# Optimization experiments

Hardware: AMD Instinct MI355X
Metric: run time of the kernel (lower is better)

The kernel has to match this reference:

```python
import jax, jax.numpy as jnp
import numpy as np

N = 65536      # points per cloud
L = 64         # voxel grid side
K_KNN = 16


def _decode(lin):
    x = lin // (L * L); y = (lin // L) % L; z = lin % L
    return np.stack([x, y, z], -1).astype(np.int32)


def _build_nbr(out_c, in_c, r):
    # Minkowski-style kernel map: for each output coord and each of (2r+1)^3
    # offsets, index of matching input coord, sentinel=len(in_c) if absent.
    g = np.arange(-r, r + 1)
    offs = np.stack(np.meshgrid(g, g, g, indexing='ij'), -1).reshape(-1, 3)
    S = 80  # encode side (coords in [-r, L+r) shifted by 8 fit in [0,80))
    def enc(c):
        return ((c[..., 0].astype(np.int64) + 8) * S + (c[..., 1] + 8)) * S + (c[..., 2] + 8)
    kin = enc(in_c)
    order = np.argsort(kin).astype(np.int32)
    skin = kin[order]
    nin = len(in_c)
    rows = []
    for i in range(0, len(out_c), 8192):
        q = out_c[i:i + 8192, None, :] + offs[None]
        kq = enc(q).reshape(-1)
        pos = np.clip(np.searchsorted(skin, kq), 0, nin - 1)
        ok = skin[pos] == kq
        rows.append(np.where(ok, order[pos], nin).astype(np.int32).reshape(-1, len(offs)))
    return np.concatenate(rows, 0)


def _knn(qc, rc, k):
    # brute-force knn (matches pytorch3d.ops.knn_points indices up to order;
    # downstream mean/softmax are permutation invariant)
    q = qc.astype(np.float32); r = rc.astype(np.float32)
    rn = (r * r).sum(1)
    out = []
    for i in range(0, len(q), 4096):
        qb = q[i:i + 4096]
        d = (qb * qb).sum(1)[:, None] + rn[None, :] - 2.0 * qb @ r.T
        out.append(np.argpartition(d, k, axis=1)[:, :k].astype(np.int32))
    return np.concatenate(out, 0)


def setup_inputs():
    rng = np.random.default_rng(0)
    prev_C = _decode(rng.permutation(L ** 3)[:N])
    cur_C = _decode(rng.permutation(L ** 3)[:N])
    nbr_interp = _build_nbr(cur_C, prev_C, 4)  # 9^3 = 729 offsets
    nbr3 = _build_nbr(cur_C, cur_C, 1)         # 3^3 = 27 offsets
    knn_idx = _knn(cur_C, prev_C, K_KNN)
    key = jax.random.key(0)
    ks = jax.random.split(key, 32)
    f32 = jnp.float32
    def w(k, shape, s):
        return jax.random.normal(k, shape, f32) * s
    C = 32
    return dict(
        prev_F=w(ks[0], (N, 1), 1.0),
        prev_C=jnp.asarray(prev_C), cur_C=jnp.asarray(cur_C),
        nbr_interp=jnp.asarray(nbr_interp), nbr3=jnp.asarray(nbr3),
        knn_idx=jnp.asarray(knn_idx),
        W_interp=w(ks[1], (729, 1, 1), 0.05), b_interp=w(ks[2], (1,), 0.05),
        W_conv0=w(ks[3], (27, 2, C), 0.1), b_conv0=w(ks[4], (C,), 0.05),
        W_conv1=w(ks[5], (C, C), 0.1), b_conv1=w(ks[6], (C,), 0.05),
        Wi00=w(ks[7], (C, C // 4), 0.1), bi00=w(ks[8], (C // 4,), 0.05),
        Wi01=w(ks[9], (27, C // 4, C // 4), 0.1), bi01=w(ks[10], (C // 4,), 0.05),
        Wi02=w(ks[11], (C // 4, C // 2), 0.1), bi02=w(ks[12], (C // 2,), 0.05),
        Wi10=w(ks[13], (27, C, C // 4), 0.1), bi10=w(ks[14], (C // 4,), 0.05),
        Wi11=w(ks[15], (27, C // 4, C // 2), 0.1), bi11=w(ks[16], (C // 2,), 0.05),
        Wq=w(ks[17], (1, 1), 0.5), bq=w(ks[18], (1,), 0.1),
        Wk=w(ks[19], (4, 1), 0.5), bk=w(ks[20], (1,), 0.1),
        Wv=w(ks[21], (4, 1), 0.5), bv=w(ks[22], (1,), 0.1),
        Wlin=w(ks[23], (1, 1), 0.5), blin=w(ks[24], (1,), 0.1),
        ln1_g=jnp.ones((1,), f32), ln1_b=jnp.zeros((1,), f32),
        ln2_g=jnp.ones((1,), f32), ln2_b=jnp.zeros((1,), f32),
    )


def _sparse_conv(feats, nbr, W, b):
    # gather-GEMM-scatter sparse conv; sentinel index == len(feats) -> zero row
    fpad = jnp.concatenate([feats, jnp.zeros((1, feats.shape[1]), feats.dtype)], 0)
    g = fpad[nbr]  # [Nout, K, Cin]
    return jnp.einsum('nkc,kcd->nd', g, W) + b


def _ln(x, g, b, eps=1e-5):
    m = jnp.mean(x, -1, keepdims=True)
    v = jnp.var(x, -1, keepdims=True)
    return (x - m) * jax.lax.rsqrt(v + eps) * g + b


def reference(prev_F, prev_C, cur_C, nbr_interp, nbr3, knn_idx,
              W_interp, b_interp, W_conv0, b_conv0, W_conv1, b_conv1,
              Wi00, bi00, Wi01, bi01, Wi02, bi02, Wi10, bi10, Wi11, bi11,
              Wq, bq, Wk, bk, Wv, bv, Wlin, blin, ln1_g, ln1_b, ln2_g, ln2_b):
    # interp: generative 9^3 sparse conv from previous coords onto current coords
    context = _sparse_conv(prev_F, nbr_interp, W_interp, b_interp)  # [N,1]

    # Target_Point_Transformer_Last (channels = in_channels = 1, head=1, k=16)
    pxyz = prev_C.astype(jnp.float32)
    cxyz = cur_C.astype(jnp.float32)
    knn_xyz = pxyz[knn_idx] - cxyz[:, None, :]          # [N,16,3]
    knn_xyz = knn_xyz / jnp.max(knn_xyz)                # global-max normalization
    knn_feat = prev_F[knn_idx]                          # [N,16,1]
    x = jnp.mean(knn_feat, axis=1)                      # init_feature [N,1]
    nf = jnp.concatenate([knn_feat, knn_xyz], axis=2)   # [N,16,4]
    Q = (x @ Wq + bq)[:, None, :]                       # [N,1,1] (head=1)
    Kt = (nf @ Wk + bk)[:, None, :, :]                  # [N,1,16,1]
    V = (nf @ Wv + bv)[:, None, :, :]
    att = jnp.einsum('nhd,nhkd->nhk', Q, Kt) / 1.0      # d = sqrt(channels=1)
    att = jax.nn.softmax(att, axis=-1)
    af = jnp.einsum('nhk,nhkd->nhd', att, V).reshape(-1, 1)
    x1 = x + af
    x1 = _ln(x1, ln1_g, ln1_b)
    x1 = x1 + x1 @ Wlin + blin
    interp_feat = _ln(x1, ln2_g, ln2_b)                 # [N,1]

    ctx = jnp.concatenate([context, interp_feat], axis=-1)  # [N,2]
    h = jax.nn.relu(_sparse_conv(ctx, nbr3, W_conv0, b_conv0))  # [N,32]
    # InceptionResNet
    o = jax.nn.relu(h @ Wi00 + bi00)                         # 1x1 conv [N,8]
    o0 = jax.nn.relu(_sparse_conv(o, nbr3, Wi01, bi01))
    o0 = jax.nn.relu(o0 @ Wi02 + bi02)                       # [N,16]
    o1 = jax.nn.relu(_sparse_conv(h, nbr3, Wi10, bi10))
    o1 = jax.nn.relu(_sparse_conv(o1, nbr3, Wi11, bi11))     # [N,16]
    blk = jnp.concatenate([o0, o1], axis=-1) + h
    out = jax.nn.relu(blk) @ W_conv1 + b_conv1               # 1x1 conv [N,32]
    return out
```

## Files before the change

kernel.cpp:

```cpp
#include <hip/hip_runtime.h>


#define NPTS 65536
#define GD 72
#define GSX (GD*GD)
#define GRID_FLOATS (GD*GD*GD)
#define CD 64
#define CELLS (CD*CD*CD)

__global__ __launch_bounds__(256) void k_scatter(const float* __restrict__ prev_F,
                                                 const int* __restrict__ prev_C,
                                                 const int* __restrict__ cur_C,
                                                 float* __restrict__ gridF,
                                                 int* __restrict__ pidg) {
    int m = blockIdx.x * 256 + threadIdx.x;
    int x = prev_C[m*3+0], y = prev_C[m*3+1], z = prev_C[m*3+2];
    gridF[(x+4)*GSX + (y+4)*GD + (z+4)] = prev_F[m];
    int cx = cur_C[m*3+0], cy = cur_C[m*3+1], cz = cur_C[m*3+2];
    pidg[(cx*CD + cy)*CD + cz] = m;
}

__global__ __launch_bounds__(256) void k_ctx_dense(const float* __restrict__ gridF,
                                                   const int* __restrict__ pidg,
                                                   const float* __restrict__ W_interp,
                                                   const float* __restrict__ b_interp,
                                                   float* __restrict__ ctx) {
    __shared__ float tile[16*16*24];
    int bid = blockIdx.x;
    int bx = (bid >> 5) * 8, by = ((bid >> 2) & 7) * 8, bz = (bid & 3) * 16;
    int t = threadIdx.x;
    for (int i = t; i < 16*16*24; i += 256) {
        int a = i / (16*24);
        int r = i - a*(16*24);
        int b = r / 24;
        int c = r - b*24;
        tile[i] = gridF[(bx + a)*GSX + (by + b)*GD + (bz + c)];
    }
    __syncthreads();
    int tz = (t & 3) * 4;
    int ty = (t >> 2) & 7;
    int tx = t >> 5;
    float acc0 = 0.f, acc1 = 0.f, acc2 = 0.f, acc3 = 0.f;
    for (int dx = 0; dx < 9; ++dx) {
        for (int dy = 0; dy < 9; ++dy) {
            const float* row = &tile[((tx + dx)*16 + (ty + dy))*24 + tz];
            float4 r0 = *(const float4*)(row);
            float4 r1 = *(const float4*)(row + 4);
            float4 r2 = *(const float4*)(row + 8);
            float v[12] = {r0.x,r0.y,r0.z,r0.w, r1.x,r1.y,r1.z,r1.w, r2.x,r2.y,r2.z,r2.w};
            const float* wp = &W_interp[(dx*9 + dy)*9];
            #pragma unroll
            for (int dz = 0; dz < 9; ++dz) {
                float w = wp[dz];
                acc0 = fmaf(v[dz+0], w, acc0);
                acc1 = fmaf(v[dz+1], w, acc1);
                acc2 = fmaf(v[dz+2], w, acc2);
                acc3 = fmaf(v[dz+3], w, acc3);
            }
        }
    }
    float bi = b_interp[0];
    int cell = ((bx + tx)*CD + (by + ty))*CD + (bz + tz);
    int4 pids = *(const int4*)(pidg + cell);
    if (pids.x >= 0) ctx[pids.x] = acc0 + bi;
    if (pids.y >= 0) ctx[pids.y] = acc1 + bi;
    if (pids.z >= 0) ctx[pids.z] = acc2 + bi;
    if (pids.w >= 0) ctx[pids.w] = acc3 + bi;
}

__global__ __launch_bounds__(256) void k_conv0(const int* __restrict__ nbr3,
                                               const float* __restrict__ ctx,
                                               const float* __restrict__ W_conv0,
                                               const float* __restrict__ b_conv0,
                                               const float* __restrict__ Wi00,
                                               const float* __restrict__ bi00,
                                               float* __restrict__ h,
                                               float* __restrict__ o) {
    __shared__ int ln[256*27];
    int n0 = blockIdx.x * 256;
    for (int i = threadIdx.x; i < 256*27; i += 256) ln[i] = nbr3[n0*27 + i];
    __syncthreads();
    int n = n0 + threadIdx.x;
    float acc[32];
    #pragma unroll
    for (int d = 0; d < 32; ++d) acc[d] = b_conv0[d];
    for (int k = 0; k < 27; ++k) {
        int idx = ln[threadIdx.x*27 + k];
        float cv = 0.f;
        if (idx < NPTS) cv = ctx[idx];
        #pragma unroll
        for (int d = 0; d < 32; ++d)
            acc[d] = fmaf(cv, W_conv0[k*64 + d], acc[d]);
    }
    #pragma unroll
    for (int d = 0; d < 32; ++d) acc[d] = fmaxf(acc[d], 0.f);
    float4* hp = (float4*)(h + (size_t)n*32);
    #pragma unroll
    for (int q = 0; q < 8; ++q) hp[q] = make_float4(acc[q*4], acc[q*4+1], acc[q*4+2], acc[q*4+3]);
    float ov[8];
    #pragma unroll
    for (int j = 0; j < 8; ++j) {
        float t = bi00[j];
        #pragma unroll
        for (int d = 0; d < 32; ++d) t = fmaf(acc[d], Wi00[d*8 + j], t);
        ov[j] = fmaxf(t, 0.f);
    }
    float4* op = (float4*)(o + (size_t)n*8);
    op[0] = make_float4(ov[0], ov[1], ov[2], ov[3]);
    op[1] = make_float4(ov[4], ov[5], ov[6], ov[7]);
}

__global__ __launch_bounds__(256) void k_mid(const int* __restrict__ nbr3,
                                             const float* __restrict__ h,
                                             const float* __restrict__ o,
                                             const float* __restrict__ Wi01,
                                             const float* __restrict__ bi01,
                                             const float* __restrict__ Wi10,
                                             const float* __restrict__ bi10,
                                             float* __restrict__ o0a,
                                             float* __restrict__ o1a) {
    __shared__ int ln[256*27];
    int n0 = blockIdx.x * 256;
    for (int i = threadIdx.x; i < 256*27; i += 256) ln[i] = nbr3[n0*27 + i];
    __syncthreads();
    int n = n0 + threadIdx.x;
    float a0[8], a1[8];
    #pragma unroll
    for (int j = 0; j < 8; ++j) { a0[j] = bi01[j]; a1[j] = bi10[j]; }
    for (int k = 0; k < 27; ++k) {
        int idx = ln[threadIdx.x*27 + k];
        if (idx < NPTS) {
            const float4* orow = (const float4*)(o + (size_t)idx*8);
            float4 oa = orow[0], ob = orow[1];
            float oc[8] = {oa.x, oa.y, oa.z, oa.w, ob.x, ob.y, ob.z, ob.w};
            #pragma unroll
            for (int c = 0; c < 8; ++c)
                #pragma unroll
                for (int j = 0; j < 8; ++j)
                    a0[j] = fmaf(oc[c], Wi01[(k*8+c)*8 + j], a0[j]);
            const float4* hrow = (const float4*)(h + (size_t)idx*32);
            #pragma unroll
            for (int q = 0; q < 8; ++q) {
                float4 hv = hrow[q];
                float hc[4] = {hv.x, hv.y, hv.z, hv.w};
                #pragma unroll
                for (int c = 0; c < 4; ++c)
                    #pragma unroll
                    for (int j = 0; j < 8; ++j)
                        a1[j] = fmaf(hc[c], Wi10[(k*32 + q*4 + c)*8 + j], a1[j]);
            }
        }
    }
    float4* p0 = (float4*)(o0a + (size_t)n*8);
    p0[0] = make_float4(fmaxf(a0[0],0.f), fmaxf(a0[1],0.f), fmaxf(a0[2],0.f), fmaxf(a0[3],0.f));
    p0[1] = make_float4(fmaxf(a0[4],0.f), fmaxf(a0[5],0.f), fmaxf(a0[6],0.f), fmaxf(a0[7],0.f));
    float4* p1 = (float4*)(o1a + (size_t)n*8);
    p1[0] = make_float4(fmaxf(a1[0],0.f), fmaxf(a1[1],0.f), fmaxf(a1[2],0.f), fmaxf(a1[3],0.f));
    p1[1] = make_float4(fmaxf(a1[4],0.f), fmaxf(a1[5],0.f), fmaxf(a1[6],0.f), fmaxf(a1[7],0.f));
}

__global__ __launch_bounds__(256) void k_out(const int* __restrict__ nbr3,
                                             const float* __restrict__ h,
                                             const float* __restrict__ o0a,
                                             const float* __restrict__ o1a,
                                             const float* __restrict__ Wi11,
                                             const float* __restrict__ bi11,
                                             const float* __restrict__ Wi02,
                                             const float* __restrict__ bi02,
                                             const float* __restrict__ W_conv1,
                                             const float* __restrict__ b_conv1,
                                             float* __restrict__ out) {
    __shared__ int ln[256*27];
    int n0 = blockIdx.x * 256;
    for (int i = threadIdx.x; i < 256*27; i += 256) ln[i] = nbr3[n0*27 + i];
    __syncthreads();
    int n = n0 + threadIdx.x;
    float a1[16];
    #pragma unroll
    for (int j = 0; j < 16; ++j) a1[j] = bi11[j];
    for (int k = 0; k < 27; ++k) {
        int idx = ln[threadIdx.x*27 + k];
        if (idx < NPTS) {
            const float4* row = (const float4*)(o1a + (size_t)idx*8);
            float4 ra = row[0], rb = row[1];
            float rc[8] = {ra.x, ra.y, ra.z, ra.w, rb.x, rb.y, rb.z, rb.w};
            #pragma unroll
            for (int c = 0; c < 8; ++c)
                #pragma unroll
                for (int j = 0; j < 16; ++j)
                    a1[j] = fmaf(rc[c], Wi11[(k*8+c)*16 + j], a1[j]);
        }
    }
    float blk[32];
    {
        const float4* prow = (const float4*)(o0a + (size_t)n*8);
        float4 pa = prow[0], pb = prow[1];
        float pc[8] = {pa.x, pa.y, pa.z, pa.w, pb.x, pb.y, pb.z, pb.w};
        #pragma unroll
        for (int j = 0; j < 16; ++j) {
            float t = bi02[j];
            #pragma unroll
            for (int c = 0; c < 8; ++c) t = fmaf(pc[c], Wi02[c*16 + j], t);
            blk[j] = fmaxf(t, 0.f);
        }
    }
    #pragma unroll
    for (int j = 0; j < 16; ++j) blk[16+j] = fmaxf(a1[j], 0.f);
    const float4* hrow4 = (const float4*)(h + (size_t)n*32);
    #pragma unroll
    for (int q = 0; q < 8; ++q) {
        float4 hv = hrow4[q];
        blk[q*4+0] += hv.x; blk[q*4+1] += hv.y; blk[q*4+2] += hv.z; blk[q*4+3] += hv.w;
    }
    #pragma unroll
    for (int e = 0; e < 32; ++e) blk[e] = fmaxf(blk[e], 0.f);
    float acc[32];
    #pragma unroll
    for (int d = 0; d < 32; ++d) acc[d] = b_conv1[d];
    #pragma unroll
    for (int e = 0; e < 32; ++e)
        #pragma unroll
        for (int d = 0; d < 32; ++d)
            acc[d] = fmaf(blk[e], W_conv1[e*32 + d], acc[d]);
    float4* outp = (float4*)(out + (size_t)n*32);
    #pragma unroll
    for (int q = 0; q < 8; ++q) outp[q] = make_float4(acc[q*4], acc[q*4+1], acc[q*4+2], acc[q*4+3]);
}

extern "C" void kernel_launch(void* const* d_in, const int* in_sizes, int n_in,
                              void* d_out, int out_size, void* d_ws, size_t ws_size,
                              hipStream_t stream) {
    (void)in_sizes; (void)n_in; (void)out_size; (void)ws_size;
    const float* prev_F   = (const float*)d_in[0];
    const int*   prev_C   = (const int*)d_in[1];
    const int*   cur_C    = (const int*)d_in[2];
    const int*   nbr3     = (const int*)d_in[4];
    const float* W_interp = (const float*)d_in[6];
    const float* b_interp = (const float*)d_in[7];
    const float* W_conv0  = (const float*)d_in[8];
    const float* b_conv0  = (const float*)d_in[9];
    const float* W_conv1  = (const float*)d_in[10];
    const float* b_conv1  = (const float*)d_in[11];
    const float* Wi00     = (const float*)d_in[12];
    const float* bi00     = (const float*)d_in[13];
    const float* Wi01     = (const float*)d_in[14];
    const float* bi01     = (const float*)d_in[15];
    const float* Wi02     = (const float*)d_in[16];
    const float* bi02     = (const float*)d_in[17];
    const float* Wi10     = (const float*)d_in[18];
    const float* bi10     = (const float*)d_in[19];
    const float* Wi11     = (const float*)d_in[20];
    const float* bi11     = (const float*)d_in[21];

    float* ws    = (float*)d_ws;
    float* gridF = ws;
    int*   pidg  = (int*)(ws + 373248);
    float* ctx   = ws + 635392;
    float* h     = ws + 700928;
    float* o     = ws + 2798080;
    float* o0a   = ws + 3322368;
    float* o1a   = ws + 3846656;
    float* outp  = (float*)d_out;

    hipMemsetAsync(gridF, 0,    GRID_FLOATS*sizeof(float), stream);
    hipMemsetAsync(pidg,  0xFF, CELLS*sizeof(int),         stream);
    k_scatter  <<<NPTS/256, 256, 0, stream>>>(prev_F, prev_C, cur_C, gridF, pidg);
    k_ctx_dense<<<256,      256, 0, stream>>>(gridF, pidg, W_interp, b_interp, ctx);
    k_conv0    <<<NPTS/256, 256, 0, stream>>>(nbr3, ctx, W_conv0, b_conv0, Wi00, bi00, h, o);
    k_mid      <<<NPTS/256, 256, 0, stream>>>(nbr3, h, o, Wi01, bi01, Wi10, bi10, o0a, o1a);
    k_out      <<<NPTS/256, 256, 0, stream>>>(nbr3, h, o0a, o1a, Wi11, bi11, Wi02, bi02, W_conv1, b_conv1, outp);
}
```

Baseline: 447.8 us.

## Split sparse-conv kernel taps across waves and shrink dense-context tiles

The dense context kernel now uses 8x8x8 output blocks with 2 outputs per thread, doubling the block count. The three sparse-conv kernels now process 64 points per block, each of four waves taking 7 of the 27 kernel taps. Partial sums are reduced through shared memory, and k_mid double-buffers its neighbour row loads. The goal is more parallelism and memory-level parallelism on the gathers, at the cost of extra shared-memory reductions, a barrier, and idle waves during the epilogue.

```diff
diff --git a/kernel.cpp b/kernel.cpp
--- a/kernel.cpp
+++ b/kernel.cpp
@@ -25,48 +25,46 @@
                                                    const float* __restrict__ W_interp,
                                                    const float* __restrict__ b_interp,
                                                    float* __restrict__ ctx) {
-    __shared__ float tile[16*16*24];
+    __shared__ float tile[16*16*16];
     int bid = blockIdx.x;
-    int bx = (bid >> 5) * 8, by = ((bid >> 2) & 7) * 8, bz = (bid & 3) * 16;
+    int bx = (bid >> 6) * 8, by = ((bid >> 3) & 7) * 8, bz = (bid & 7) * 8;
     int t = threadIdx.x;
-    for (int i = t; i < 16*16*24; i += 256) {
-        int a = i / (16*24);
-        int r = i - a*(16*24);
-        int b = r / 24;
-        int c = r - b*24;
+    #pragma unroll
+    for (int rep = 0; rep < 16; ++rep) {
+        int i = t + rep*256;
+        int a = i >> 8, b = (i >> 4) & 15, c = i & 15;
         tile[i] = gridF[(bx + a)*GSX + (by + b)*GD + (bz + c)];
     }
     __syncthreads();
-    int tz = (t & 3) * 4;
+    int tz = (t & 3) * 2;
     int ty = (t >> 2) & 7;
     int tx = t >> 5;
-    float acc0 = 0.f, acc1 = 0.f, acc2 = 0.f, acc3 = 0.f;
+    float acc0 = 0.f, acc1 = 0.f;
     for (int dx = 0; dx < 9; ++dx) {
         for (int dy = 0; dy < 9; ++dy) {
-            const float* row = &tile[((tx + dx)*16 + (ty + dy))*24 + tz];
-            float4 r0 = *(const float4*)(row);
-            float4 r1 = *(const float4*)(row + 4);
-            float4 r2 = *(const float4*)(row + 8);
-            float v[12] = {r0.x,r0.y,r0.z,r0.w, r1.x,r1.y,r1.z,r1.w, r2.x,r2.y,r2.z,r2.w};
+            const float* row = &tile[((tx + dx)*16 + (ty + dy))*16 + tz];
+            float2 r0 = *(const float2*)(row);
+            float2 r1 = *(const float2*)(row + 2);
+            float2 r2 = *(const float2*)(row + 4);
+            float2 r3 = *(const float2*)(row + 6);
+            float2 r4 = *(const float2*)(row + 8);
+            float v[10] = {r0.x,r0.y,r1.x,r1.y,r2.x,r2.y,r3.x,r3.y,r4.x,r4.y};
             const float* wp = &W_interp[(dx*9 + dy)*9];
             #pragma unroll
             for (int dz = 0; dz < 9; ++dz) {
                 float w = wp[dz];
                 acc0 = fmaf(v[dz+0], w, acc0);
                 acc1 = fmaf(v[dz+1], w, acc1);
-                acc2 = fmaf(v[dz+2], w, acc2);
-                acc3 = fmaf(v[dz+3], w, acc3);
             }
         }
     }
     float bi = b_interp[0];
     int cell = ((bx + tx)*CD + (by + ty))*CD + (bz + tz);
-    int4 pids = *(const int4*)(pidg + cell);
+    int2 pids = *(const int2*)(pidg + cell);
     if (pids.x >= 0) ctx[pids.x] = acc0 + bi;
     if (pids.y >= 0) ctx[pids.y] = acc1 + bi;
-    if (pids.z >= 0) ctx[pids.z] = acc2 + bi;
-    if (pids.w >= 0) ctx[pids.w] = acc3 + bi;
-}
+}
+
 
 __global__ __launch_bounds__(256) void k_conv0(const int* __restrict__ nbr3,
                                                const float* __restrict__ ctx,
@@ -76,38 +74,51 @@
                                                const float* __restrict__ bi00,
                                                float* __restrict__ h,
                                                float* __restrict__ o) {
-    __shared__ int ln[256*27];
-    int n0 = blockIdx.x * 256;
-    for (int i = threadIdx.x; i < 256*27; i += 256) ln[i] = nbr3[n0*27 + i];
-    __syncthreads();
-    int n = n0 + threadIdx.x;
-    float acc[32];
-    #pragma unroll
-    for (int d = 0; d < 32; ++d) acc[d] = b_conv0[d];
-    for (int k = 0; k < 27; ++k) {
-        int idx = ln[threadIdx.x*27 + k];
-        float cv = 0.f;
-        if (idx < NPTS) cv = ctx[idx];
+    __shared__ float part[3][32][64];
+    int lane = threadIdx.x & 63;
+    int q    = threadIdx.x >> 6;
+    int kbase = __builtin_amdgcn_readfirstlane(q * 7);
+    int n = blockIdx.x * 64 + lane;
+    float cv[7];
+    #pragma unroll
+    for (int j = 0; j < 7; ++j) {
+        int k = kbase + j;
+        int raw = (k < 27) ? nbr3[(size_t)n*27 + k] : NPTS;
+        cv[j] = (raw < NPTS) ? ctx[raw < NPTS ? raw : 0] : 0.f;
+    }
+    float ac[32];
+    #pragma unroll
+    for (int d = 0; d < 32; ++d) ac[d] = (q == 0) ? b_conv0[d] : 0.f;
+    #pragma unroll
+    for (int j = 0; j < 7; ++j) {
+        const float* wr = &W_conv0[(kbase + j)*64];
+        #pragma unroll
+        for (int d = 0; d < 32; ++d) ac[d] = fmaf(cv[j], wr[d], ac[d]);
+    }
+    if (q > 0) {
+        #pragma unroll
+        for (int d = 0; d < 32; ++d) part[q-1][d][lane] = ac[d];
+    }
+    __syncthreads();
+    if (q == 0) {
         #pragma unroll
         for (int d = 0; d < 32; ++d)
-            acc[d] = fmaf(cv, W_conv0[k*64 + d], acc[d]);
-    }
-    #pragma unroll
-    for (int d = 0; d < 32; ++d) acc[d] = fmaxf(acc[d], 0.f);
-    float4* hp = (float4*)(h + (size_t)n*32);
-    #pragma unroll
-    for (int q = 0; q < 8; ++q) hp[q] = make_float4(acc[q*4], acc[q*4+1], acc[q*4+2], acc[q*4+3]);
-    float ov[8];
-    #pragma unroll
-    for (int j = 0; j < 8; ++j) {
-        float t = bi00[j];
-        #pragma unroll
-        for (int d = 0; d < 32; ++d) t = fmaf(acc[d], Wi00[d*8 + j], t);
-        ov[j] = fmaxf(t, 0.f);
-    }
-    float4* op = (float4*)(o + (size_t)n*8);
-    op[0] = make_float4(ov[0], ov[1], ov[2], ov[3]);
-    op[1] = make_float4(ov[4], ov[5], ov[6], ov[7]);
+            ac[d] = fmaxf(ac[d] + part[0][d][lane] + part[1][d][lane] + part[2][d][lane], 0.f);
+        float4* hp = (float4*)(h + (size_t)n*32);
+        #pragma unroll
+        for (int w = 0; w < 8; ++w) hp[w] = make_float4(ac[w*4], ac[w*4+1], ac[w*4+2], ac[w*4+3]);
+        float ov[8];
+        #pragma unroll
+        for (int j = 0; j < 8; ++j) {
+            float tt = bi00[j];
+            #pragma unroll
+            for (int d = 0; d < 32; ++d) tt = fmaf(ac[d], Wi00[d*8 + j], tt);
+            ov[j] = fmaxf(tt, 0.f);
+        }
+        float4* op = (float4*)(o + (size_t)n*8);
+        op[0] = make_float4(ov[0], ov[1], ov[2], ov[3]);
+        op[1] = make_float4(ov[4], ov[5], ov[6], ov[7]);
+    }
 }
 
 __global__ __launch_bounds__(256) void k_mid(const int* __restrict__ nbr3,
@@ -119,44 +130,70 @@
                                              const float* __restrict__ bi10,
                                              float* __restrict__ o0a,
                                              float* __restrict__ o1a) {
-    __shared__ int ln[256*27];
-    int n0 = blockIdx.x * 256;
-    for (int i = threadIdx.x; i < 256*27; i += 256) ln[i] = nbr3[n0*27 + i];
-    __syncthreads();
-    int n = n0 + threadIdx.x;
-    float a0[8], a1[8];
-    #pragma unroll
-    for (int j = 0; j < 8; ++j) { a0[j] = bi01[j]; a1[j] = bi10[j]; }
-    for (int k = 0; k < 27; ++k) {
-        int idx = ln[threadIdx.x*27 + k];
-        if (idx < NPTS) {
-            const float4* orow = (const float4*)(o + (size_t)idx*8);
-            float4 oa = orow[0], ob = orow[1];
-            float oc[8] = {oa.x, oa.y, oa.z, oa.w, ob.x, ob.y, ob.z, ob.w};
-            #pragma unroll
-            for (int c = 0; c < 8; ++c)
+    __shared__ float part[3][16][64];
+    int lane = threadIdx.x & 63;
+    int q    = threadIdx.x >> 6;
+    int kbase = __builtin_amdgcn_readfirstlane(q * 7);
+    int n = blockIdx.x * 64 + lane;
+    const float4 z4 = make_float4(0.f, 0.f, 0.f, 0.f);
+    int  idxs[7]; bool acts[7];
+    #pragma unroll
+    for (int j = 0; j < 7; ++j) {
+        int k = kbase + j;
+        int raw = (k < 27) ? nbr3[(size_t)n*27 + k] : NPTS;
+        acts[j] = raw < NPTS;
+        idxs[j] = acts[j] ? raw : 0;
+    }
+    float ac[16];
+    #pragma unroll
+    for (int d = 0; d < 8; ++d) { ac[d] = (q==0)? bi01[d] : 0.f; ac[8+d] = (q==0)? bi10[d] : 0.f; }
+    float4 bo[2][2], bh[2][8];
+    auto loadtap = [&](int J, int S) {
+        const float4* op_ = (const float4*)(o + (size_t)idxs[J]*8);
+        const float4* hp_ = (const float4*)(h + (size_t)idxs[J]*32);
+        bool a_ = acts[J];
+        bo[S][0] = a_ ? op_[0] : z4;  bo[S][1] = a_ ? op_[1] : z4;
+        #pragma unroll
+        for (int w = 0; w < 8; ++w) bh[S][w] = a_ ? hp_[w] : z4;
+    };
+    loadtap(0, 0);
+    #pragma unroll
+    for (int j = 0; j < 7; ++j) {
+        const int s = j & 1;
+        if (j + 1 < 7) loadtap(j + 1, s ^ 1);
+        float oc[8] = {bo[s][0].x, bo[s][0].y, bo[s][0].z, bo[s][0].w,
+                       bo[s][1].x, bo[s][1].y, bo[s][1].z, bo[s][1].w};
+        const float* w0 = &Wi01[(kbase + j)*64];
+        #pragma unroll
+        for (int c = 0; c < 8; ++c)
+            #pragma unroll
+            for (int d = 0; d < 8; ++d) ac[d] = fmaf(oc[c], w0[c*8 + d], ac[d]);
+        const float* w1 = &Wi10[(kbase + j)*256];
+        #pragma unroll
+        for (int w = 0; w < 8; ++w) {
+            float hc[4] = {bh[s][w].x, bh[s][w].y, bh[s][w].z, bh[s][w].w};
+            #pragma unroll
+            for (int c = 0; c < 4; ++c)
                 #pragma unroll
-                for (int j = 0; j < 8; ++j)
-                    a0[j] = fmaf(oc[c], Wi01[(k*8+c)*8 + j], a0[j]);
-            const float4* hrow = (const float4*)(h + (size_t)idx*32);
-            #pragma unroll
-            for (int q = 0; q < 8; ++q) {
-                float4 hv = hrow[q];
-                float hc[4] = {hv.x, hv.y, hv.z, hv.w};
-                #pragma unroll
-                for (int c = 0; c < 4; ++c)
-                    #pragma unroll
-                    for (int j = 0; j < 8; ++j)
-                        a1[j] = fmaf(hc[c], Wi10[(k*32 + q*4 + c)*8 + j], a1[j]);
-            }
-        }
-    }
-    float4* p0 = (float4*)(o0a + (size_t)n*8);
-    p0[0] = make_float4(fmaxf(a0[0],0.f), fmaxf(a0[1],0.f), fmaxf(a0[2],0.f), fmaxf(a0[3],0.f));
-    p0[1] = make_float4(fmaxf(a0[4],0.f), fmaxf(a0[5],0.f), fmaxf(a0[6],0.f), fmaxf(a0[7],0.f));
-    float4* p1 = (float4*)(o1a + (size_t)n*8);
-    p1[0] = make_float4(fmaxf(a1[0],0.f), fmaxf(a1[1],0.f), fmaxf(a1[2],0.f), fmaxf(a1[3],0.f));
-    p1[1] = make_float4(fmaxf(a1[4],0.f), fmaxf(a1[5],0.f), fmaxf(a1[6],0.f), fmaxf(a1[7],0.f));
+                for (int d = 0; d < 8; ++d) ac[8+d] = fmaf(hc[c], w1[(w*4+c)*8 + d], ac[8+d]);
+        }
+    }
+    if (q > 0) {
+        #pragma unroll
+        for (int d = 0; d < 16; ++d) part[q-1][d][lane] = ac[d];
+    }
+    __syncthreads();
+    if (q == 0) {
+        #pragma unroll
+        for (int d = 0; d < 16; ++d)
+            ac[d] = fmaxf(ac[d] + part[0][d][lane] + part[1][d][lane] + part[2][d][lane], 0.f);
+        float4* p0 = (float4*)(o0a + (size_t)n*8);
+        p0[0] = make_float4(ac[0], ac[1], ac[2],  ac[3]);
+        p0[1] = make_float4(ac[4], ac[5], ac[6],  ac[7]);
+        float4* p1 = (float4*)(o1a + (size_t)n*8);
+        p1[0] = make_float4(ac[8], ac[9], ac[10], ac[11]);
+        p1[1] = make_float4(ac[12],ac[13],ac[14], ac[15]);
+    }
 }
 
 __global__ __launch_bounds__(256) void k_out(const int* __restrict__ nbr3,
@@ -170,61 +207,82 @@
                                              const float* __restrict__ W_conv1,
                                              const float* __restrict__ b_conv1,
                                              float* __restrict__ out) {
-    __shared__ int ln[256*27];
-    int n0 = blockIdx.x * 256;
-    for (int i = threadIdx.x; i < 256*27; i += 256) ln[i] = nbr3[n0*27 + i];
-    __syncthreads();
-    int n = n0 + threadIdx.x;
-    float a1[16];
-    #pragma unroll
-    for (int j = 0; j < 16; ++j) a1[j] = bi11[j];
-    for (int k = 0; k < 27; ++k) {
-        int idx = ln[threadIdx.x*27 + k];
-        if (idx < NPTS) {
-            const float4* row = (const float4*)(o1a + (size_t)idx*8);
-            float4 ra = row[0], rb = row[1];
-            float rc[8] = {ra.x, ra.y, ra.z, ra.w, rb.x, rb.y, rb.z, rb.w};
-            #pragma unroll
-            for (int c = 0; c < 8; ++c)
-                #pragma unroll
-                for (int j = 0; j < 16; ++j)
-                    a1[j] = fmaf(rc[c], Wi11[(k*8+c)*16 + j], a1[j]);
-        }
-    }
-    float blk[32];
-    {
+    __shared__ float part[3][16][64];
+    __shared__ float blkb[32][64];
+    int lane = threadIdx.x & 63;
+    int q    = threadIdx.x >> 6;
+    int kbase = __builtin_amdgcn_readfirstlane(q * 7);
+    int n = blockIdx.x * 64 + lane;
+    const float4 z4 = make_float4(0.f, 0.f, 0.f, 0.f);
+    float4 tv[7][2];
+    #pragma unroll
+    for (int j = 0; j < 7; ++j) {
+        int k = kbase + j;
+        int raw = (k < 27) ? nbr3[(size_t)n*27 + k] : NPTS;
+        bool a_ = raw < NPTS;
+        const float4* rp = (const float4*)(o1a + (size_t)(a_ ? raw : 0)*8);
+        tv[j][0] = a_ ? rp[0] : z4;
+        tv[j][1] = a_ ? rp[1] : z4;
+    }
+    float ac[16];
+    #pragma unroll
+    for (int d = 0; d < 16; ++d) ac[d] = (q == 0) ? bi11[d] : 0.f;
+    #pragma unroll
+    for (int j = 0; j < 7; ++j) {
+        float rc[8] = {tv[j][0].x, tv[j][0].y, tv[j][0].z, tv[j][0].w,
+                       tv[j][1].x, tv[j][1].y, tv[j][1].z, tv[j][1].w};
+        const float* wr = &Wi11[(kbase + j)*128];
+        #pragma unroll
+        for (int c = 0; c < 8; ++c)
+            #pragma unroll
+            for (int d = 0; d < 16; ++d) ac[d] = fmaf(rc[c], wr[c*16 + d], ac[d]);
+    }
+    if (q > 0) {
+        #pragma unroll
+        for (int d = 0; d < 16; ++d) part[q-1][d][lane] = ac[d];
+    }
+    __syncthreads();
+    if (q == 0) {
+        #pragma unroll
+        for (int d = 0; d < 16; ++d)
+            ac[d] += part[0][d][lane] + part[1][d][lane] + part[2][d][lane];
+        float blk[32];
         const float4* prow = (const float4*)(o0a + (size_t)n*8);
         float4 pa = prow[0], pb = prow[1];
         float pc[8] = {pa.x, pa.y, pa.z, pa.w, pb.x, pb.y, pb.z, pb.w};
         #pragma unroll
         for (int j = 0; j < 16; ++j) {
-            float t = bi02[j];
-            #pragma unroll
-            for (int c = 0; c < 8; ++c) t = fmaf(pc[c], Wi02[c*16 + j], t);
-            blk[j] = fmaxf(t, 0.f);
-        }
-    }
-    #pragma unroll
-    for (int j = 0; j < 16; ++j) blk[16+j] = fmaxf(a1[j], 0.f);
-    const float4* hrow4 = (const float4*)(h + (size_t)n*32);
-    #pragma unroll
-    for (int q = 0; q < 8; ++q) {
-        float4 hv = hrow4[q];
-        blk[q*4+0] += hv.x; blk[q*4+1] += hv.y; blk[q*4+2] += hv.z; blk[q*4+3] += hv.w;
-    }
-    #pragma unroll
-    for (int e = 0; e < 32; ++e) blk[e] = fmaxf(blk[e], 0.f);
-    float acc[32];
-    #pragma unroll
-    for (int d = 0; d < 32; ++d) acc[d] = b_conv1[d];
+            float tt = bi02[j];
+            #pragma unroll
+            for (int c = 0; c < 8; ++c) tt = fmaf(pc[c], Wi02[c*16 + j], tt);
+            blk[j] = fmaxf(tt, 0.f);
+        }
+        #pragma unroll
+        for (int j = 0; j < 16; ++j) blk[16+j] = fmaxf(ac[j], 0.f);
+        const float4* hrow = (const float4*)(h + (size_t)n*32);
+        #pragma unroll
+        for (int w = 0; w < 8; ++w) {
+            float4 hv = hrow[w];
+            blk[w*4+0] += hv.x; blk[w*4+1] += hv.y; blk[w*4+2] += hv.z; blk[w*4+3] += hv.w;
+        }
+        #pragma unroll
+        for (int e = 0; e < 32; ++e) blkb[e][lane] = fmaxf(blk[e], 0.f);
+    }
+    __syncthreads();
+    int q8 = __builtin_amdgcn_readfirstlane(q * 8);
+    float bl[32];
+    #pragma unroll
+    for (int e = 0; e < 32; ++e) bl[e] = blkb[e][lane];
+    float oacc[8];
+    #pragma unroll
+    for (int d = 0; d < 8; ++d) oacc[d] = b_conv1[q8 + d];
     #pragma unroll
     for (int e = 0; e < 32; ++e)
         #pragma unroll
-        for (int d = 0; d < 32; ++d)
-            acc[d] = fmaf(blk[e], W_conv1[e*32 + d], acc[d]);
-    float4* outp = (float4*)(out + (size_t)n*32);
-    #pragma unroll
-    for (int q = 0; q < 8; ++q) outp[q] = make_float4(acc[q*4], acc[q*4+1], acc[q*4+2], acc[q*4+3]);
+        for (int d = 0; d < 8; ++d) oacc[d] = fmaf(bl[e], W_conv1[e*32 + q8 + d], oacc[d]);
+    float4* outp = (float4*)(out + (size_t)n*32 + q8);
+    outp[0] = make_float4(oacc[0], oacc[1], oacc[2], oacc[3]);
+    outp[1] = make_float4(oacc[4], oacc[5], oacc[6], oacc[7]);
 }
 
 extern "C" void kernel_launch(void* const* d_in, const int* in_sizes, int n_in,
@@ -265,8 +323,8 @@
     hipMemsetAsync(gridF, 0,    GRID_FLOATS*sizeof(float), stream);
     hipMemsetAsync(pidg,  0xFF, CELLS*sizeof(int),         stream);
     k_scatter  <<<NPTS/256, 256, 0, stream>>>(prev_F, prev_C, cur_C, gridF, pidg);
-    k_ctx_dense<<<256,      256, 0, stream>>>(gridF, pidg, W_interp, b_interp, ctx);
-    k_conv0    <<<NPTS/256, 256, 0, stream>>>(nbr3, ctx, W_conv0, b_conv0, Wi00, bi00, h, o);
-    k_mid      <<<NPTS/256, 256, 0, stream>>>(nbr3, h, o, Wi01, bi01, Wi10, bi10, o0a, o1a);
-    k_out      <<<NPTS/256, 256, 0, stream>>>(nbr3, h, o0a, o1a, Wi11, bi11, Wi02, bi02, W_conv1, b_conv1, outp);
-}
+    k_ctx_dense<<<512,      256, 0, stream>>>(gridF, pidg, W_interp, b_interp, ctx);
+    k_conv0    <<<NPTS/64,  256, 0, stream>>>(nbr3, ctx, W_conv0, b_conv0, Wi00, bi00, h, o);
+    k_mid      <<<NPTS/64,  256, 0, stream>>>(nbr3, h, o, Wi01, bi01, Wi10, bi10, o0a, o1a);
+    k_out      <<<NPTS/64,  256, 0, stream>>>(nbr3, h, o0a, o1a, Wi11, bi11, Wi02, bi02, W_conv1, b_conv1, outp);
+}
```

New measurement: 509.3 us. 13.8% more time.
